# Performance work log

Hardware: AMD Instinct MI355X
Metric: run time of the kernel (lower is better)

The kernel has to match this reference:

```python
import jax, jax.numpy as jnp
import numpy as np

B, C, H, W = 8, 128, 64, 64


def conv1x1(x, w, b):
    # x: [B,C,H,W], w: [Cout,Cin], b: [Cout] -> [B,Cout,H,W]
    return jnp.einsum('bchw,oc->bohw', x, w) + b[None, :, None, None]


def setup_inputs() -> dict:
    key = jax.random.key(0)
    ks = jax.random.split(key, 8)
    scale = 1.0 / np.sqrt(C)  # keep QK logits in a sane range
    return {
        'cur': jax.random.normal(ks[0], (B, C, H, W), jnp.float32),
        'ref': jax.random.normal(ks[1], (B, C, H, W), jnp.float32),
        'theta_w': jax.random.normal(ks[2], (C, C), jnp.float32) * scale,
        'theta_b': jnp.zeros((C,), jnp.float32),
        'phi_w': jax.random.normal(ks[3], (C, C), jnp.float32) * scale,
        'phi_b': jnp.zeros((C,), jnp.float32),
        'W_w': jax.random.normal(ks[4], (C, C), jnp.float32) * scale,
        'W_b': jnp.zeros((C,), jnp.float32),
    }


def reference(cur, ref, theta_w, theta_b, phi_w, phi_b, W_w, W_b):
    b, c, h, w = cur.shape
    n = h * w
    # x = theta(ref): [B, N, C]  (queries come from the reference frame)
    x = conv1x1(ref, theta_w, theta_b).reshape(b, c, n).transpose(0, 2, 1)
    # y = phi(cur): [B, C, N]
    y = conv1x1(cur, phi_w, phi_b).reshape(b, c, n)
    # attn: [B, N_ref, N_cur], softmax over the NON-standard axis 1 (ref positions)
    attn = jax.nn.softmax(jnp.einsum('bnc,bcm->bnm', x, y), axis=1)
    # z = attn @ x: [B, N, C] -> [B, C, H, W]
    z = jnp.einsum('bnm,bmc->bnc', attn, x).transpose(0, 2, 1).reshape(b, c, h, w)
    return conv1x1(z, W_w, W_b)
```

## Files before the change

kernel.cpp:

```cpp
#include <hip/hip_runtime.h>
#include <hip/hip_bf16.h>

#define BB 8
#define CC 128
#define NN 4096
#define LOG2E 1.44269504088896340736f

typedef __attribute__((ext_vector_type(8))) short bf16x8;
typedef __attribute__((ext_vector_type(16))) float f32x16;

static __device__ __forceinline__ unsigned short f2bfu(float f) {
  unsigned int x = __float_as_uint(f);
  x += 0x7fffu + ((x >> 16) & 1u);
  return (unsigned short)(x >> 16);
}
static __device__ __forceinline__ unsigned int packbf(float a, float b) {
  return (unsigned int)f2bfu(a) | ((unsigned int)f2bfu(b) << 16);
}
static __device__ __forceinline__ float bfu2f(unsigned short u) {
  return __uint_as_float((unsigned int)u << 16);
}
static __device__ __forceinline__ float fexp2(float x) {
  return __builtin_amdgcn_exp2f(x);
}
static __device__ __forceinline__ f32x16 zero16() {
  f32x16 z;
#pragma unroll
  for (int i = 0; i < 16; ++i) z[i] = 0.f;
  return z;
}
union Frag { int i[4]; unsigned int u[4]; bf16x8 v; };

static __device__ __forceinline__ unsigned int cvtpk(float a, float b) {
  unsigned int r;
  asm("v_cvt_pk_bf16_f32 %0, %1, %2" : "=v"(r) : "v"(a), "v"(b));
  return r;
}
static __device__ __forceinline__ void pl32swap(unsigned int& d, unsigned int& s) {
  asm volatile("v_permlane32_swap_b32 %0, %1" : "+v"(d), "+v"(s));
}

#define GLD16(gp, lp)                                                     \
  __builtin_amdgcn_global_load_lds(                                       \
      (const __attribute__((address_space(1))) unsigned int*)(gp),        \
      (__attribute__((address_space(3))) unsigned int*)(lp), 16, 0, 0)

#define ROWPAT(rg, q2) (((rg) & 3) + 8 * ((rg) >> 2) + 4 * (q2))

static __device__ __forceinline__ void make_pa(const f32x16& s, Frag& lo, Frag& hi) {
  float p[16];
#pragma unroll
  for (int rg = 0; rg < 16; ++rg) p[rg] = fexp2(s[rg]);
  unsigned int a0 = cvtpk(p[0], p[1]),   b0 = cvtpk(p[4], p[5]);
  pl32swap(a0, b0);
  unsigned int a1 = cvtpk(p[2], p[3]),   b1 = cvtpk(p[6], p[7]);
  pl32swap(a1, b1);
  lo.u[0] = a0; lo.u[1] = a1; lo.u[2] = b0; lo.u[3] = b1;
  unsigned int c0 = cvtpk(p[8], p[9]),   d0 = cvtpk(p[12], p[13]);
  pl32swap(c0, d0);
  unsigned int c1 = cvtpk(p[10], p[11]), d1 = cvtpk(p[14], p[15]);
  pl32swap(c1, d1);
  hi.u[0] = c0; hi.u[1] = c1; hi.u[2] = d0; hi.u[3] = d1;
}

__global__ __launch_bounds__(256, 4) void nl_conv2m(
    const float* __restrict__ ref, const float* __restrict__ theta_w,
    const float* __restrict__ theta_b,
    const float* __restrict__ cur, const float* __restrict__ phi_w,
    const float* __restrict__ phi_b,
    unsigned short* __restrict__ Xnc, unsigned short* __restrict__ Xcn,
    unsigned short* __restrict__ Ync)
{
  __shared__ float sm[64 * 129];
  const int z  = blockIdx.z;
  const float* in   = z ? cur : ref;
  const float* w    = z ? phi_w : theta_w;
  const float* bias = z ? phi_b : theta_b;
  unsigned short* out_nc = z ? Ync : Xnc;
  unsigned short* out_cn = z ? nullptr : Xcn;
  const float nc_scale = z ? 1.0f : LOG2E;

  const int b  = blockIdx.y;
  const int n0 = blockIdx.x * 64;
  const int t  = threadIdx.x;
  const int wave = t >> 6, lane = t & 63, q2 = lane >> 5, cm = lane & 31;

#pragma unroll
  for (int k = 0; k < 16; ++k) {
    int flat = t + 256 * k;
    int c = flat >> 5, jp = flat & 31;
    float2 v = *(const float2*)&in[(size_t)b * CC * NN + (size_t)c * NN + n0 + jp * 2];
    sm[c * 64 + jp * 2]     = v.x;
    sm[c * 64 + jp * 2 + 1] = v.y;
  }

  bf16x8 wf[8];
  const int o0 = wave * 32 + cm;
#pragma unroll
  for (int k = 0; k < 8; ++k) {
    const float* wp = &w[o0 * CC + k * 16 + q2 * 8];
    float4 w0 = *(const float4*)wp, w1 = *(const float4*)(wp + 4);
    Frag f;
    f.u[0] = packbf(w0.x, w0.y); f.u[1] = packbf(w0.z, w0.w);
    f.u[2] = packbf(w1.x, w1.y); f.u[3] = packbf(w1.z, w1.w);
    wf[k] = f.v;
  }
  __syncthreads();

  f32x16 acc[2];
  acc[0] = zero16(); acc[1] = zero16();
#pragma unroll
  for (int k = 0; k < 8; ++k) {
#pragma unroll
    for (int jt = 0; jt < 2; ++jt) {
      int base = (k * 16 + q2 * 8) * 64 + jt * 32 + cm;
      Frag xb;
      xb.u[0] = cvtpk(sm[base],       sm[base + 64]);
      xb.u[1] = cvtpk(sm[base + 128], sm[base + 192]);
      xb.u[2] = cvtpk(sm[base + 256], sm[base + 320]);
      xb.u[3] = cvtpk(sm[base + 384], sm[base + 448]);
      acc[jt] = __builtin_amdgcn_mfma_f32_32x32x16_bf16(wf[k], xb.v, acc[jt], 0, 0, 0);
    }
  }
  __syncthreads();

#pragma unroll
  for (int jt = 0; jt < 2; ++jt)
#pragma unroll
    for (int rg = 0; rg < 16; ++rg) {
      int o = wave * 32 + ROWPAT(rg, q2);
      sm[(jt * 32 + cm) * 129 + o] = acc[jt][rg] + bias[o];
    }
  __syncthreads();

#pragma unroll
  for (int k = 0; k < 16; ++k) {
    int flat = t + 256 * k;
    int cp = flat & 63, jj = flat >> 6;
    float f0 = sm[jj * 129 + cp * 2] * nc_scale;
    float f1 = sm[jj * 129 + cp * 2 + 1] * nc_scale;
    *(unsigned int*)(out_nc + ((size_t)b * NN + n0 + jj) * CC + cp * 2) = packbf(f0, f1);
  }
  if (out_cn) {
#pragma unroll
    for (int k = 0; k < 16; ++k) {
      int flat = t + 256 * k;
      int jp = flat & 31, c = flat >> 5;
      float f0 = sm[(jp * 2) * 129 + c], f1 = sm[(jp * 2 + 1) * 129 + c];
      *(unsigned int*)(out_cn + ((size_t)b * CC + c) * NN + n0 + jp * 2) = packbf(f0, f1);
    }
  }
}

__global__ __launch_bounds__(256, 4) void nl_stats4(
    const unsigned short* __restrict__ Xnc, const unsigned short* __restrict__ Ync,
    float* __restrict__ Lpart)
{
  __shared__ unsigned short Xt[2][64 * 128];
  __shared__ float sL[2][2][2][32];
  const int b = blockIdx.z, nq = blockIdx.y, mstrip = blockIdx.x;
  const int t = threadIdx.x;
  const int wave = t >> 6, lane = t & 63, q2 = lane >> 5, cm = lane & 31;
  const int mq = wave & 1, nh = wave >> 1;
  const int m0w = mstrip * 128 + mq * 64;

  bf16x8 bf[2][8];
#pragma unroll
  for (int ct = 0; ct < 2; ++ct)
#pragma unroll
    for (int k = 0; k < 8; ++k)
      bf[ct][k] = *(const bf16x8*)(Ync + ((size_t)b * NN + m0w + ct * 32 + cm) * CC + k * 16 + q2 * 8);

  {
    const int n0 = nq * 1024;
#pragma unroll
    for (int i = 0; i < 4; ++i) {
      int slot = i * 256 + t;
      int row = slot >> 4, g = (slot & 15) ^ (row & 15);
      GLD16(Xnc + ((size_t)b * NN + n0 + row) * CC + g * 8, &Xt[0][0] + i * 2048 + wave * 512);
    }
  }

  float runL[2] = {0.f, 0.f};
#pragma unroll 2
  for (int nt = 0; nt < 16; ++nt) {
    __syncthreads();
    if (nt < 15) {
      const int n0 = nq * 1024 + (nt + 1) * 64;
      unsigned short* dst = &Xt[(nt + 1) & 1][0];
#pragma unroll
      for (int i = 0; i < 4; ++i) {
        int slot = i * 256 + t;
        int row = slot >> 4, g = (slot & 15) ^ (row & 15);
        GLD16(Xnc + ((size_t)b * NN + n0 + row) * CC + g * 8, dst + i * 2048 + wave * 512);
      }
    }
    const unsigned short* src = &Xt[nt & 1][0];
    f32x16 acc0 = zero16(), acc1 = zero16();
#pragma unroll
    for (int k = 0; k < 8; ++k) {
      bf16x8 av = *(const bf16x8*)&src[(nh * 32 + cm) * 128 + (((k << 1) | q2) ^ (cm & 15)) * 8];
      acc0 = __builtin_amdgcn_mfma_f32_32x32x16_bf16(av, bf[0][k], acc0, 0, 0, 0);
      acc1 = __builtin_amdgcn_mfma_f32_32x32x16_bf16(av, bf[1][k], acc1, 0, 0, 0);
    }
#pragma unroll
    for (int rg = 0; rg < 16; ++rg) {
      runL[0] += fexp2(acc0[rg]);
      runL[1] += fexp2(acc1[rg]);
    }
  }
#pragma unroll
  for (int ct = 0; ct < 2; ++ct) runL[ct] += __shfl_xor(runL[ct], 32);
  if (q2 == 0) {
    sL[nh][mq][0][cm] = runL[0];
    sL[nh][mq][1][cm] = runL[1];
  }
  __syncthreads();
  if (t < 128) {
    int mq2 = t >> 6, ct2 = (t >> 5) & 1, cm2 = t & 31;
    float L = sL[0][mq2][ct2][cm2] + sL[1][mq2][ct2][cm2];
    Lpart[((size_t)nq * BB + b) * NN + mstrip * 128 + mq2 * 64 + ct2 * 32 + cm2] = L;
  }
}

__global__ __launch_bounds__(256) void nl_scalev(
    const float* __restrict__ Lp, unsigned short* __restrict__ Xcn)
{
  __shared__ float iL[64];
  const int b = blockIdx.y, mc = blockIdx.x;
  const int t = threadIdx.x;
  const int m0 = mc * 64;
  if (t < 64) {
    size_t idx = (size_t)b * NN + m0 + t;
    float L = Lp[idx] + Lp[(size_t)BB * NN + idx] + Lp[(size_t)2 * BB * NN + idx] +
              Lp[(size_t)3 * BB * NN + idx];
    iL[t] = 1.0f / L;
  }
  __syncthreads();
#pragma unroll
  for (int r = 0; r < 4; ++r) {
    int idx = r * 256 + t;
    int c = idx >> 3, mg = idx & 7;
    size_t base = ((size_t)b * CC + c) * NN + m0 + mg * 8;
    Frag x; x.v = *(const bf16x8*)(Xcn + base);
    const float* il = &iL[mg * 8];
    Frag o;
    o.u[0] = packbf(bfu2f(x.u[0] & 0xffff) * il[0], bfu2f(x.u[0] >> 16) * il[1]);
    o.u[1] = packbf(bfu2f(x.u[1] & 0xffff) * il[2], bfu2f(x.u[1] >> 16) * il[3]);
    o.u[2] = packbf(bfu2f(x.u[2] & 0xffff) * il[4], bfu2f(x.u[2] >> 16) * il[5]);
    o.u[3] = packbf(bfu2f(x.u[3] & 0xffff) * il[6], bfu2f(x.u[3] >> 16) * il[7]);
    *(bf16x8*)(Xcn + base) = o.v;
  }
}

__global__ __launch_bounds__(256, 2) void nl_pass2e2(
    const unsigned short* __restrict__ Xnc, const unsigned short* __restrict__ Ync,
    const unsigned short* __restrict__ Xsc,
    unsigned short* __restrict__ Zpart)
{
  __shared__ unsigned short Yt[2][64 * 128];
  __shared__ unsigned short Xv[2][128 * 64];
  const int b = blockIdx.z, mhalf = blockIdx.y, nstrip = blockIdx.x;
  const int t = threadIdx.x;
  const int wave = t >> 6, lane = t & 63, q2 = lane >> 5, cm = lane & 31;

  bf16x8 af[8];
#pragma unroll
  for (int k = 0; k < 8; ++k)
    af[k] = *(const bf16x8*)(Xnc +
        ((size_t)b * NN + nstrip * 128 + wave * 32 + cm) * CC + k * 16 + q2 * 8);

  f32x16 z[4];
#pragma unroll
  for (int ct = 0; ct < 4; ++ct) z[ct] = zero16();

  {
    const int m0g = mhalf * 2048;
#pragma unroll
    for (int i = 0; i < 4; ++i) {
      int slot = i * 256 + t;
      int row = slot >> 4, g = (slot & 15) ^ (row & 15);
      GLD16(Ync + ((size_t)b * NN + m0g + row) * CC + g * 8, &Yt[0][0] + i * 2048 + wave * 512);
    }
#pragma unroll
    for (int i = 0; i < 4; ++i) {
      int slot = i * 256 + t;
      int row = slot >> 3, g = (slot & 7) ^ (row & 7);
      GLD16(Xsc + ((size_t)b * CC + row) * NN + m0g + g * 8, &Xv[0][0] + i * 2048 + wave * 512);
    }
  }

#define P2_ITER(BUF, MT)                                                       \
  do {                                                                         \
    __syncthreads();                                                           \
    if ((MT) < 31) {                                                           \
      const int m0g = mhalf * 2048 + ((MT) + 1) * 64;                          \
      unsigned short* Yd = &Yt[(BUF) ^ 1][0];                                  \
      unsigned short* Xd = &Xv[(BUF) ^ 1][0];                                  \
      _Pragma("unroll")                                                        \
      for (int i = 0; i < 4; ++i) {                                            \
        int slot = i * 256 + t;                                                \
        int row = slot >> 4, g = (slot & 15) ^ (row & 15);                     \
        GLD16(Ync + ((size_t)b * NN + m0g + row) * CC + g * 8,                 \
              Yd + i * 2048 + wave * 512);                                     \
      }                                                                        \
      _Pragma("unroll")                                                        \
      for (int i = 0; i < 4; ++i) {                                            \
        int slot = i * 256 + t;                                                \
        int row = slot >> 3, g = (slot & 7) ^ (row & 7);                       \
        GLD16(Xsc + ((size_t)b * CC + row) * NN + m0g + g * 8,                 \
              Xd + i * 2048 + wave * 512);                                     \
      }                                                                        \
    }                                                                          \
    const unsigned short* Ys = &Yt[BUF][0];                                    \
    f32x16 s0 = zero16(), s1 = zero16();                                       \
    __builtin_amdgcn_s_setprio(1);                                             \
    _Pragma("unroll")                                                          \
    for (int k = 0; k < 8; ++k) {                                              \
      const int ch = (((k << 1) | q2) ^ (cm & 15)) * 8;                        \
      bf16x8 av0 = *(const bf16x8*)&Ys[cm * 128 + ch];                         \
      bf16x8 av1 = *(const bf16x8*)&Ys[(32 + cm) * 128 + ch];                  \
      s0 = __builtin_amdgcn_mfma_f32_32x32x16_bf16(av0, af[k], s0, 0, 0, 0);   \
      s1 = __builtin_amdgcn_mfma_f32_32x32x16_bf16(av1, af[k], s1, 0, 0, 0);   \
    }                                                                          \
    __builtin_amdgcn_s_setprio(0);                                             \
    Frag pa[4];                                                                \
    make_pa(s0, pa[0], pa[1]);                                                 \
    make_pa(s1, pa[2], pa[3]);                                                 \
    const unsigned short* Xs = &Xv[BUF][0];                                    \
    __builtin_amdgcn_s_setprio(1);                                             \
    _Pragma("unroll")                                                          \
    for (int ks = 0; ks < 4; ++ks) {                                           \
      const int ch = (((ks << 1) | q2) ^ (cm & 7)) * 8;                        \
      _Pragma("unroll")                                                        \
      for (int ct = 0; ct < 4; ++ct) {                                         \
        bf16x8 xv = *(const bf16x8*)&Xs[(ct * 32 + cm) * 64 + ch];             \
        z[ct] = __builtin_amdgcn_mfma_f32_32x32x16_bf16(pa[ks].v, xv, z[ct], 0, 0, 0); \
      }                                                                        \
    }                                                                          \
    __builtin_amdgcn_s_setprio(0);                                             \
  } while (0)

  for (int mt2 = 0; mt2 < 16; ++mt2) {
    P2_ITER(0, mt2 * 2);
    P2_ITER(1, mt2 * 2 + 1);
  }
#undef P2_ITER

  unsigned short* Zp = Zpart + ((size_t)mhalf * BB + b) * NN * CC;
#pragma unroll
  for (int ct = 0; ct < 4; ++ct)
#pragma unroll
    for (int rg = 0; rg < 16; ++rg) {
      int n = nstrip * 128 + wave * 32 + ROWPAT(rg, q2);
      Zp[(size_t)n * CC + ct * 32 + cm] = f2bfu(z[ct][rg]);
    }
}

__global__ __launch_bounds__(256) void nl_convw2(
    const unsigned short* __restrict__ Zpart, const float* __restrict__ w,
    const float* __restrict__ bias, float* __restrict__ out)
{
  __shared__ unsigned short Zt[64 * 128];
  const int b = blockIdx.y, nstrip = blockIdx.x;
  const int t = threadIdx.x;
  const int wave = t >> 6, lane = t & 63, q2 = lane >> 5, cm = lane & 31;
  const int oh = wave & 1, nh2 = wave >> 1;

  const unsigned short* Z0 = Zpart + ((size_t)b * NN + nstrip * 64) * CC;
  const unsigned short* Z1 = Z0 + (size_t)BB * NN * CC;
#pragma unroll
  for (int i = 0; i < 4; ++i) {
    int slot = i * 256 + t;
    int row = slot >> 4, g = slot & 15;
    size_t off = (size_t)row * CC + g * 8;
    Frag a, c2, o;
    a.v  = *(const bf16x8*)(Z0 + off);
    c2.v = *(const bf16x8*)(Z1 + off);
#pragma unroll
    for (int w2 = 0; w2 < 4; ++w2) {
      float lo = bfu2f((unsigned short)(a.u[w2] & 0xffff)) +
                 bfu2f((unsigned short)(c2.u[w2] & 0xffff));
      float hi = bfu2f((unsigned short)(a.u[w2] >> 16)) +
                 bfu2f((unsigned short)(c2.u[w2] >> 16));
      o.u[w2] = packbf(lo, hi);
    }
    *(bf16x8*)&Zt[row * 128 + ((g ^ (row & 7)) * 8)] = o.v;
  }

  bf16x8 wf[2][8];
#pragma unroll
  for (int s2 = 0; s2 < 2; ++s2)
#pragma unroll
    for (int k = 0; k < 8; ++k) {
      const float* wp = &w[(oh * 64 + s2 * 32 + cm) * CC + k * 16 + q2 * 8];
      float4 w0 = *(const float4*)wp, w1 = *(const float4*)(wp + 4);
      Frag f;
      f.u[0] = packbf(w0.x, w0.y); f.u[1] = packbf(w0.z, w0.w);
      f.u[2] = packbf(w1.x, w1.y); f.u[3] = packbf(w1.z, w1.w);
      wf[s2][k] = f.v;
    }
  __syncthreads();

  f32x16 z[2];
  z[0] = zero16(); z[1] = zero16();
#pragma unroll
  for (int k = 0; k < 8; ++k) {
    bf16x8 bv = *(const bf16x8*)&Zt[(nh2 * 32 + cm) * 128 + (((k << 1) | q2) ^ (cm & 7)) * 8];
#pragma unroll
    for (int i = 0; i < 2; ++i)
      z[i] = __builtin_amdgcn_mfma_f32_32x32x16_bf16(wf[i][k], bv, z[i], 0, 0, 0);
  }

#pragma unroll
  for (int i = 0; i < 2; ++i)
#pragma unroll
    for (int rg = 0; rg < 16; ++rg) {
      int o = oh * 64 + i * 32 + ROWPAT(rg, q2);
      int n = nstrip * 64 + nh2 * 32 + cm;
      out[(size_t)b * CC * NN + (size_t)o * NN + n] = z[i][rg] + bias[o];
    }
}

extern "C" void kernel_launch(void* const* d_in, const int* in_sizes, int n_in,
                              void* d_out, int out_size, void* d_ws, size_t ws_size,
                              hipStream_t stream) {
  const float* cur     = (const float*)d_in[0];
  const float* ref     = (const float*)d_in[1];
  const float* theta_w = (const float*)d_in[2];
  const float* theta_b = (const float*)d_in[3];
  const float* phi_w   = (const float*)d_in[4];
  const float* phi_b   = (const float*)d_in[5];
  const float* Ww      = (const float*)d_in[6];
  const float* Wb      = (const float*)d_in[7];
  float* out = (float*)d_out;

  unsigned short* Xnc = (unsigned short*)d_ws;
  unsigned short* Ync = Xnc + (size_t)BB * NN * CC;
  unsigned short* Xcn = Ync + (size_t)BB * NN * CC;
  float* Lpart = (float*)(Xcn + (size_t)BB * NN * CC);
  unsigned short* Zpart = (unsigned short*)(Lpart + (size_t)4 * BB * NN);

  dim3 blk(256);
  nl_conv2m  <<<dim3(64, BB, 2), blk, 0, stream>>>(ref, theta_w, theta_b,
                                                   cur, phi_w, phi_b, Xnc, Xcn, Ync);
  nl_stats4  <<<dim3(32, 4, BB), blk, 0, stream>>>(Xnc, Ync, Lpart);
  nl_scalev  <<<dim3(64, BB), blk, 0, stream>>>(Lpart, Xcn);
  nl_pass2e2 <<<dim3(32, 2, BB), blk, 0, stream>>>(Xnc, Ync, Xcn, Zpart);
  nl_convw2  <<<dim3(64, BB), blk, 0, stream>>>(Zpart, Ww, Wb, out);
}
```

Baseline: 233.3 us.

## Fuse softmax normalization into pass2 and drop separate scale kernel

Removes the nl_scalev kernel that rescaled Xcn by 1/L in place. Each pass2 block now sums the four partial L values for its 2048 columns, stores the reciprocals in LDS, and multiplies them into the exponentiated probabilities before the bf16 pack. This saves one kernel launch and a full read-modify-write of Xcn, at the cost of extra LDS, per-block redundant L loads and more ALU work in the inner loop. The Zt swizzle in the final conv also widens from 8 to 16 groups to cut bank conflicts.

```diff
diff --git a/kernel.cpp b/kernel.cpp
--- a/kernel.cpp
+++ b/kernel.cpp
@@ -47,10 +47,21 @@
 
 #define ROWPAT(rg, q2) (((rg) & 3) + 8 * ((rg) >> 2) + 4 * (q2))
 
-static __device__ __forceinline__ void make_pa(const f32x16& s, Frag& lo, Frag& hi) {
+static __device__ __forceinline__ void make_pa_s(
+    const f32x16& s, const float* il, int q2, Frag& lo, Frag& hi) {
+  const float4 i0 = *(const float4*)&il[4 * q2];
+  const float4 i1 = *(const float4*)&il[4 * q2 + 8];
+  const float4 i2 = *(const float4*)&il[4 * q2 + 16];
+  const float4 i3 = *(const float4*)&il[4 * q2 + 24];
   float p[16];
-#pragma unroll
-  for (int rg = 0; rg < 16; ++rg) p[rg] = fexp2(s[rg]);
+  p[0]  = fexp2(s[0])  * i0.x; p[1]  = fexp2(s[1])  * i0.y;
+  p[2]  = fexp2(s[2])  * i0.z; p[3]  = fexp2(s[3])  * i0.w;
+  p[4]  = fexp2(s[4])  * i1.x; p[5]  = fexp2(s[5])  * i1.y;
+  p[6]  = fexp2(s[6])  * i1.z; p[7]  = fexp2(s[7])  * i1.w;
+  p[8]  = fexp2(s[8])  * i2.x; p[9]  = fexp2(s[9])  * i2.y;
+  p[10] = fexp2(s[10]) * i2.z; p[11] = fexp2(s[11]) * i2.w;
+  p[12] = fexp2(s[12]) * i3.x; p[13] = fexp2(s[13]) * i3.y;
+  p[14] = fexp2(s[14]) * i3.z; p[15] = fexp2(s[15]) * i3.w;
   unsigned int a0 = cvtpk(p[0], p[1]),   b0 = cvtpk(p[4], p[5]);
   pl32swap(a0, b0);
   unsigned int a1 = cvtpk(p[2], p[3]),   b1 = cvtpk(p[6], p[7]);
@@ -223,43 +234,14 @@
   }
 }
 
-__global__ __launch_bounds__(256) void nl_scalev(
-    const float* __restrict__ Lp, unsigned short* __restrict__ Xcn)
-{
-  __shared__ float iL[64];
-  const int b = blockIdx.y, mc = blockIdx.x;
-  const int t = threadIdx.x;
-  const int m0 = mc * 64;
-  if (t < 64) {
-    size_t idx = (size_t)b * NN + m0 + t;
-    float L = Lp[idx] + Lp[(size_t)BB * NN + idx] + Lp[(size_t)2 * BB * NN + idx] +
-              Lp[(size_t)3 * BB * NN + idx];
-    iL[t] = 1.0f / L;
-  }
-  __syncthreads();
-#pragma unroll
-  for (int r = 0; r < 4; ++r) {
-    int idx = r * 256 + t;
-    int c = idx >> 3, mg = idx & 7;
-    size_t base = ((size_t)b * CC + c) * NN + m0 + mg * 8;
-    Frag x; x.v = *(const bf16x8*)(Xcn + base);
-    const float* il = &iL[mg * 8];
-    Frag o;
-    o.u[0] = packbf(bfu2f(x.u[0] & 0xffff) * il[0], bfu2f(x.u[0] >> 16) * il[1]);
-    o.u[1] = packbf(bfu2f(x.u[1] & 0xffff) * il[2], bfu2f(x.u[1] >> 16) * il[3]);
-    o.u[2] = packbf(bfu2f(x.u[2] & 0xffff) * il[4], bfu2f(x.u[2] >> 16) * il[5]);
-    o.u[3] = packbf(bfu2f(x.u[3] & 0xffff) * il[6], bfu2f(x.u[3] >> 16) * il[7]);
-    *(bf16x8*)(Xcn + base) = o.v;
-  }
-}
-
-__global__ __launch_bounds__(256, 2) void nl_pass2e2(
+__global__ __launch_bounds__(256, 2) void nl_pass2e3(
     const unsigned short* __restrict__ Xnc, const unsigned short* __restrict__ Ync,
-    const unsigned short* __restrict__ Xsc,
+    const unsigned short* __restrict__ Xcn, const float* __restrict__ Lpart,
     unsigned short* __restrict__ Zpart)
 {
   __shared__ unsigned short Yt[2][64 * 128];
   __shared__ unsigned short Xv[2][128 * 64];
+  __shared__ float iLs[2048];
   const int b = blockIdx.z, mhalf = blockIdx.y, nstrip = blockIdx.x;
   const int t = threadIdx.x;
   const int wave = t >> 6, lane = t & 63, q2 = lane >> 5, cm = lane & 31;
@@ -286,7 +268,15 @@
     for (int i = 0; i < 4; ++i) {
       int slot = i * 256 + t;
       int row = slot >> 3, g = (slot & 7) ^ (row & 7);
-      GLD16(Xsc + ((size_t)b * CC + row) * NN + m0g + g * 8, &Xv[0][0] + i * 2048 + wave * 512);
+      GLD16(Xcn + ((size_t)b * CC + row) * NN + m0g + g * 8, &Xv[0][0] + i * 2048 + wave * 512);
+    }
+    const float* Lp0 = Lpart + (size_t)b * NN + m0g;
+#pragma unroll
+    for (int i = 0; i < 8; ++i) {
+      int ml = i * 256 + t;
+      float L = Lp0[ml] + Lp0[(size_t)BB * NN + ml] +
+                Lp0[(size_t)2 * BB * NN + ml] + Lp0[(size_t)3 * BB * NN + ml];
+      iLs[ml] = 1.0f / L;
     }
   }
 
@@ -308,7 +298,7 @@
       for (int i = 0; i < 4; ++i) {                                            \
         int slot = i * 256 + t;                                                \
         int row = slot >> 3, g = (slot & 7) ^ (row & 7);                       \
-        GLD16(Xsc + ((size_t)b * CC + row) * NN + m0g + g * 8,                 \
+        GLD16(Xcn + ((size_t)b * CC + row) * NN + m0g + g * 8,                 \
               Xd + i * 2048 + wave * 512);                                     \
       }                                                                        \
     }                                                                          \
@@ -325,8 +315,8 @@
     }                                                                          \
     __builtin_amdgcn_s_setprio(0);                                             \
     Frag pa[4];                                                                \
-    make_pa(s0, pa[0], pa[1]);                                                 \
-    make_pa(s1, pa[2], pa[3]);                                                 \
+    make_pa_s(s0, &iLs[(MT) * 64],      q2, pa[0], pa[1]);                     \
+    make_pa_s(s1, &iLs[(MT) * 64 + 32], q2, pa[2], pa[3]);                     \
     const unsigned short* Xs = &Xv[BUF][0];                                    \
     __builtin_amdgcn_s_setprio(1);                                             \
     _Pragma("unroll")                                                          \
@@ -385,7 +375,7 @@
                  bfu2f((unsigned short)(c2.u[w2] >> 16));
       o.u[w2] = packbf(lo, hi);
     }
-    *(bf16x8*)&Zt[row * 128 + ((g ^ (row & 7)) * 8)] = o.v;
+    *(bf16x8*)&Zt[row * 128 + ((g ^ (row & 15)) * 8)] = o.v;
   }
 
   bf16x8 wf[2][8];
@@ -406,7 +396,7 @@
   z[0] = zero16(); z[1] = zero16();
 #pragma unroll
   for (int k = 0; k < 8; ++k) {
-    bf16x8 bv = *(const bf16x8*)&Zt[(nh2 * 32 + cm) * 128 + (((k << 1) | q2) ^ (cm & 7)) * 8];
+    bf16x8 bv = *(const bf16x8*)&Zt[(nh2 * 32 + cm) * 128 + (((k << 1) | q2) ^ (cm & 15)) * 8];
 #pragma unroll
     for (int i = 0; i < 2; ++i)
       z[i] = __builtin_amdgcn_mfma_f32_32x32x16_bf16(wf[i][k], bv, z[i], 0, 0, 0);
@@ -445,7 +435,6 @@
   nl_conv2m  <<<dim3(64, BB, 2), blk, 0, stream>>>(ref, theta_w, theta_b,
                                                    cur, phi_w, phi_b, Xnc, Xcn, Ync);
   nl_stats4  <<<dim3(32, 4, BB), blk, 0, stream>>>(Xnc, Ync, Lpart);
-  nl_scalev  <<<dim3(64, BB), blk, 0, stream>>>(Lpart, Xcn);
-  nl_pass2e2 <<<dim3(32, 2, BB), blk, 0, stream>>>(Xnc, Ync, Xcn, Zpart);
+  nl_pass2e3 <<<dim3(32, 2, BB), blk, 0, stream>>>(Xnc, Ync, Xcn, Lpart, Zpart);
   nl_convw2  <<<dim3(64, BB), blk, 0, stream>>>(Zpart, Ww, Wb, out);
 }
```

Result: no change. 231.0 us (-1.0%).
